# Kernel optimization log

Hardware: AMD Instinct MI355X
Metric: run time of the kernel (lower is better)

Reference implementation:

```python
import jax, jax.numpy as jnp
import numpy as np

B, T, D = 64, 256, 1024
H, HS = 16, 64
FF = 4096
EPS = 1e-5


def _layernorm(x, g, b):
    mu = jnp.mean(x, axis=-1, keepdims=True)
    var = jnp.mean(jnp.square(x - mu), axis=-1, keepdims=True)
    return (x - mu) * jax.lax.rsqrt(var + EPS) * g + b


def setup_inputs() -> dict:
    key = jax.random.key(0)
    ks = jax.random.split(key, 12)
    s = 0.02
    return {
        "x": jax.random.normal(ks[0], (B, T, D), jnp.float32),
        "ln1_g": jnp.ones((D,), jnp.float32),
        "ln1_b": jnp.zeros((D,), jnp.float32),
        "Wq": jax.random.normal(ks[1], (H, D, HS), jnp.float32) * s,
        "Wk": jax.random.normal(ks[2], (H, D, HS), jnp.float32) * s,
        "Wv": jax.random.normal(ks[3], (H, D, HS), jnp.float32) * s,
        "Wproj": jax.random.normal(ks[4], (D, D), jnp.float32) * s,
        "bproj": jnp.zeros((D,), jnp.float32),
        "ln2_g": jnp.ones((D,), jnp.float32),
        "ln2_b": jnp.zeros((D,), jnp.float32),
        "W1": jax.random.normal(ks[5], (D, FF), jnp.float32) * s,
        "b1": jnp.zeros((FF,), jnp.float32),
        "W2": jax.random.normal(ks[6], (FF, D), jnp.float32) * s,
        "b2": jnp.zeros((D,), jnp.float32),
    }


def reference(x, ln1_g, ln1_b, Wq, Wk, Wv, Wproj, bproj, ln2_g, ln2_b, W1, b1, W2, b2):
    # x = ln1(x)
    h = _layernorm(x, ln1_g, ln1_b)
    # per-head Q/K/V projections, batched over heads
    q = jnp.einsum("btd,hde->bhte", h, Wq)
    k = jnp.einsum("btd,hde->bhte", h, Wk)
    v = jnp.einsum("btd,hde->bhte", h, Wv)
    # NOTE: source scales by C**-0.5 with C = input_size (D), not head_size
    scale = D ** -0.5
    scores = jnp.einsum("bhte,bhse->bhts", q, k) * scale
    causal = jnp.tril(jnp.ones((T, T), bool))
    scores = jnp.where(causal, scores, -jnp.inf)
    w = jax.nn.softmax(scores, axis=-1)  # dropout is identity in eval
    attn = jnp.einsum("bhts,bhse->bthe", w, v).reshape(x.shape[0], x.shape[1], H * HS)
    sa = attn @ Wproj + bproj
    # residual onto ln1 output (as written in source)
    y = h + sa
    h2 = _layernorm(y, ln2_g, ln2_b)
    ff = jax.nn.relu(h2 @ W1 + b1) @ W2 + b2
    return h2 + ff
```

## Files before the change

### kernel.cpp

```cpp
#include <hip/hip_runtime.h>

typedef __bf16 bf16x8 __attribute__((ext_vector_type(8)));
typedef float f32x4 __attribute__((ext_vector_type(4)));
typedef unsigned short ushort_t;

__device__ __forceinline__ ushort_t f2bf(float f) {
  unsigned int u = __float_as_uint(f);
  u += 0x7fffu + ((u >> 16) & 1u);
  return (ushort_t)(u >> 16);
}

__device__ __forceinline__ void gl_lds16(const ushort_t* g, const char* l) {
  __builtin_amdgcn_global_load_lds(
      (const __attribute__((address_space(1))) void*)g,
      (__attribute__((address_space(3))) void*)l, 16, 0, 0);
}

__global__ __launch_bounds__(256) void fill_k(float* __restrict__ p, long n, float v) {
  long i = (long)blockIdx.x * 256 + threadIdx.x;
  if (i < n) p[i] = v;
}

__global__ __launch_bounds__(256) void transpose_w(const float* __restrict__ in,
                                                   ushort_t* __restrict__ out,
                                                   int R, int C) {
  __shared__ float tile[32][33];
  const float* inb = in + (long)blockIdx.z * R * C;
  ushort_t* outb = out + (long)blockIdx.z * R * C;
  int r0 = blockIdx.x * 32, c0 = blockIdx.y * 32;
  int tx = threadIdx.x & 31, ty = threadIdx.x >> 5;
#pragma unroll
  for (int i = ty; i < 32; i += 8) tile[i][tx] = inb[(long)(r0 + i) * C + (c0 + tx)];
  __syncthreads();
#pragma unroll
  for (int i = ty; i < 32; i += 8) outb[(long)(c0 + i) * R + (r0 + tx)] = f2bf(tile[tx][i]);
}

__global__ __launch_bounds__(256) void ln_k(const float* __restrict__ x,
                                            const float* __restrict__ g,
                                            const float* __restrict__ b,
                                            float* __restrict__ outF,
                                            ushort_t* __restrict__ outU) {
  __shared__ float red[8];
  long row = blockIdx.x;
  int tid = threadIdx.x;
  float4 v = ((const float4*)(x + row * 1024))[tid];
  float s = v.x + v.y + v.z + v.w;
#pragma unroll
  for (int off = 32; off; off >>= 1) s += __shfl_xor(s, off);
  int w = tid >> 6;
  if ((tid & 63) == 0) red[w] = s;
  __syncthreads();
  float mean = (red[0] + red[1] + red[2] + red[3]) * (1.0f / 1024.0f);
  float dx = v.x - mean, dy = v.y - mean, dz = v.z - mean, dw = v.w - mean;
  float s2 = dx * dx + dy * dy + dz * dz + dw * dw;
#pragma unroll
  for (int off = 32; off; off >>= 1) s2 += __shfl_xor(s2, off);
  if ((tid & 63) == 0) red[4 + w] = s2;
  __syncthreads();
  float var = (red[4] + red[5] + red[6] + red[7]) * (1.0f / 1024.0f);
  float rstd = rsqrtf(var + 1e-5f);
  int c = tid * 4;
  float o0 = dx * rstd * g[c + 0] + b[c + 0];
  float o1 = dy * rstd * g[c + 1] + b[c + 1];
  float o2 = dz * rstd * g[c + 2] + b[c + 2];
  float o3 = dw * rstd * g[c + 3] + b[c + 3];
  ((float4*)(outF + row * 1024))[tid] = make_float4(o0, o1, o2, o3);
  ushort4 u;
  u.x = f2bf(o0); u.y = f2bf(o1); u.z = f2bf(o2); u.w = f2bf(o3);
  ((ushort4*)(outU + row * 1024))[tid] = u;
}

template <int EPI>
__global__ __launch_bounds__(512, 2) void gemm256(const ushort_t* __restrict__ A,
                                                  const ushort_t* __restrict__ Bt,
                                                  int M, int N, int K, int NBC,
                                                  const float* __restrict__ bias,
                                                  const float* res, float* outF,
                                                  ushort_t* __restrict__ outU,
                                                  ushort_t* __restrict__ outU2,
                                                  ushort_t* __restrict__ outU3) {
  __shared__ __align__(16) char lds[131072];
  const int tid = threadIdx.x;
  const int lane = tid & 63;
  const int w = tid >> 6;
  const int wr = w >> 2, wc = w & 3;
  const int g = lane >> 4, lr = lane & 15;
  const int cpx = gridDim.x >> 3;
  const int wg = (blockIdx.x & 7) * cpx + (blockIdx.x >> 3);
  const long m0 = (long)(wg / NBC) * 256;
  const long n0 = (long)(wg % NBC) * 256;
  const int srow = tid >> 3;
  const int sslot = (tid & 7) ^ (srow & 7);
  const ushort_t* sA = A + (m0 + srow) * (long)K + sslot * 8;
  const ushort_t* sB = Bt + (n0 + srow) * (long)K + sslot * 8;
  const int dA = tid * 16;
  const int dB = 32768 + tid * 16;
  const int abase = (wr * 128 + lr) * 128;
  const int bbase = 32768 + (wc * 64 + lr) * 128;
  const int s0 = g ^ (lr & 7);
  const int s1 = (4 + g) ^ (lr & 7);
  const int NT = K >> 6;

  f32x4 acc[8][4] = {};

#pragma unroll
  for (int j = 0; j < 4; ++j) gl_lds16(sA + (long)j * 64 * K, lds + j * 8192 + dA);
#pragma unroll
  for (int j = 0; j < 4; ++j) gl_lds16(sB + (long)j * 64 * K, lds + j * 8192 + dB);

  bf16x8 aR[4][2], bR[4][2];
  int c = 0;
  for (int t = 0; t < NT; ++t) {
    const char* rb = lds + c;
    if (t + 1 < NT) {
      const long ko = (long)(t + 1) * 64;
      const int d = c ^ 65536;
#pragma unroll
      for (int j = 0; j < 4; ++j) gl_lds16(sA + ko + (long)j * 64 * K, lds + d + j * 8192 + dA);
#pragma unroll
      for (int j = 0; j < 4; ++j) gl_lds16(sB + ko + (long)j * 64 * K, lds + d + j * 8192 + dB);
      asm volatile("s_waitcnt vmcnt(8)" ::: "memory");
    } else {
      asm volatile("s_waitcnt vmcnt(0)" ::: "memory");
    }
    __builtin_amdgcn_s_barrier();
    __builtin_amdgcn_sched_barrier(0);
#pragma unroll
    for (int mf = 0; mf < 4; ++mf) {
      aR[mf][0] = *(const bf16x8*)(rb + abase + mf * 2048 + s0 * 16);
      aR[mf][1] = *(const bf16x8*)(rb + abase + mf * 2048 + s1 * 16);
    }
#pragma unroll
    for (int nf = 0; nf < 2; ++nf) {
      bR[nf][0] = *(const bf16x8*)(rb + bbase + nf * 2048 + s0 * 16);
      bR[nf][1] = *(const bf16x8*)(rb + bbase + nf * 2048 + s1 * 16);
    }
    __builtin_amdgcn_s_setprio(1);
#pragma unroll
    for (int mf = 0; mf < 4; ++mf)
#pragma unroll
      for (int nf = 0; nf < 2; ++nf) {
        acc[mf][nf] = __builtin_amdgcn_mfma_f32_16x16x32_bf16(aR[mf][0], bR[nf][0], acc[mf][nf], 0, 0, 0);
        acc[mf][nf] = __builtin_amdgcn_mfma_f32_16x16x32_bf16(aR[mf][1], bR[nf][1], acc[mf][nf], 0, 0, 0);
      }
    __builtin_amdgcn_s_setprio(0);
    __builtin_amdgcn_s_barrier();
#pragma unroll
    for (int nf = 2; nf < 4; ++nf) {
      bR[nf][0] = *(const bf16x8*)(rb + bbase + nf * 2048 + s0 * 16);
      bR[nf][1] = *(const bf16x8*)(rb + bbase + nf * 2048 + s1 * 16);
    }
    __builtin_amdgcn_s_setprio(1);
#pragma unroll
    for (int mf = 0; mf < 4; ++mf)
#pragma unroll
      for (int nf = 2; nf < 4; ++nf) {
        acc[mf][nf] = __builtin_amdgcn_mfma_f32_16x16x32_bf16(aR[mf][0], bR[nf][0], acc[mf][nf], 0, 0, 0);
        acc[mf][nf] = __builtin_amdgcn_mfma_f32_16x16x32_bf16(aR[mf][1], bR[nf][1], acc[mf][nf], 0, 0, 0);
      }
    __builtin_amdgcn_s_setprio(0);
    __builtin_amdgcn_s_barrier();
#pragma unroll
    for (int mf = 0; mf < 4; ++mf) {
      aR[mf][0] = *(const bf16x8*)(rb + abase + (4 + mf) * 2048 + s0 * 16);
      aR[mf][1] = *(const bf16x8*)(rb + abase + (4 + mf) * 2048 + s1 * 16);
    }
    __builtin_amdgcn_s_setprio(1);
#pragma unroll
    for (int mf = 0; mf < 4; ++mf)
#pragma unroll
      for (int nf = 2; nf < 4; ++nf) {
        acc[4 + mf][nf] = __builtin_amdgcn_mfma_f32_16x16x32_bf16(aR[mf][0], bR[nf][0], acc[4 + mf][nf], 0, 0, 0);
        acc[4 + mf][nf] = __builtin_amdgcn_mfma_f32_16x16x32_bf16(aR[mf][1], bR[nf][1], acc[4 + mf][nf], 0, 0, 0);
      }
    __builtin_amdgcn_s_setprio(0);
    __builtin_amdgcn_s_barrier();
    __builtin_amdgcn_s_setprio(1);
#pragma unroll
    for (int mf = 0; mf < 4; ++mf)
#pragma unroll
      for (int nf = 0; nf < 2; ++nf) {
        acc[4 + mf][nf] = __builtin_amdgcn_mfma_f32_16x16x32_bf16(aR[mf][0], bR[nf][0], acc[4 + mf][nf], 0, 0, 0);
        acc[4 + mf][nf] = __builtin_amdgcn_mfma_f32_16x16x32_bf16(aR[mf][1], bR[nf][1], acc[4 + mf][nf], 0, 0, 0);
      }
    __builtin_amdgcn_s_setprio(0);
    __builtin_amdgcn_s_barrier();
    c ^= 65536;
  }

#pragma unroll
  for (int mf = 0; mf < 8; ++mf)
#pragma unroll
    for (int nf = 0; nf < 4; ++nf)
#pragma unroll
      for (int r = 0; r < 4; ++r) {
        long row = m0 + wr * 128 + mf * 16 + g * 4 + r;
        long col = n0 + wc * 64 + nf * 16 + lr;
        float v = acc[mf][nf][r];
        if constexpr (EPI == 2) {
          long i = row * N + col;
          outF[i] = v + bias[col] + res[i];
        } else if constexpr (EPI == 3) {
          outU[row * N + col] = f2bf(fmaxf(v + bias[col], 0.0f));
        } else {
          long bb2 = row >> 8, tt = row & 255;
          long p = col >> 10, cc = col & 1023, hh = cc >> 6, e = cc & 63;
          if (p == 0)
            outU[(((bb2 * 16 + hh) * 256 + tt) << 6) + e] = f2bf(v);
          else if (p == 1)
            outU2[(((bb2 * 16 + hh) * 256 + tt) << 6) + e] = f2bf(v);
          else
            outU3[(((bb2 * 16 + hh) * 64 + e) << 8) + tt] = f2bf(v);
        }
      }
}

__global__ __launch_bounds__(64) void attn_k(const ushort_t* __restrict__ q,
                                             const ushort_t* __restrict__ k,
                                             const ushort_t* __restrict__ vt,
                                             ushort_t* __restrict__ ao) {
  __shared__ __align__(16) ushort_t Ps[64][40];
  const int lane = threadIdx.x;
  const int g = lane >> 4, lr = lane & 15;
  const int blk = blockIdx.x;
  const int q4 = blk & 3;
  const int bh = blk >> 2;
  const int bb = bh >> 4, hh = bh & 15;
  const int q0 = q4 * 64;
  const ushort_t* qb = q + (long)bh * 256 * 64;
  const ushort_t* kb = k + (long)bh * 256 * 64;
  const ushort_t* vb = vt + (long)bh * 64 * 256;
  bf16x8 qf[4][2];
#pragma unroll
  for (int m = 0; m < 4; m++)
#pragma unroll
    for (int ks = 0; ks < 2; ks++)
      qf[m][ks] = *(const bf16x8*)(qb + (q0 + m * 16 + lr) * 64 + ks * 32 + g * 8);
  f32x4 o[4][4] = {};
  float mrow[4][4], lrow[4][4];
#pragma unroll
  for (int m = 0; m < 4; m++)
#pragma unroll
    for (int r = 0; r < 4; r++) { mrow[m][r] = -__builtin_inff(); lrow[m][r] = 0.0f; }
  const float scale = 0.03125f;
  const int nkb = q0 / 32 + 2;
  for (int kbk = 0; kbk < nkb; kbk++) {
    f32x4 s[4][2] = {};
#pragma unroll
    for (int ks = 0; ks < 2; ks++) {
      bf16x8 kf[2];
#pragma unroll
      for (int n = 0; n < 2; n++)
        kf[n] = *(const bf16x8*)(kb + (kbk * 32 + n * 16 + lr) * 64 + ks * 32 + g * 8);
#pragma unroll
      for (int m = 0; m < 4; m++)
#pragma unroll
        for (int n = 0; n < 2; n++)
          s[m][n] = __builtin_amdgcn_mfma_f32_16x16x32_bf16(qf[m][ks], kf[n], s[m][n], 0, 0, 0);
    }
#pragma unroll
    for (int m = 0; m < 4; m++)
#pragma unroll
      for (int n = 0; n < 2; n++)
#pragma unroll
        for (int r = 0; r < 4; r++) {
          int row = q0 + m * 16 + g * 4 + r;
          int col = kbk * 32 + n * 16 + lr;
          float v = s[m][n][r] * scale;
          s[m][n][r] = (col <= row) ? v : -1e30f;
        }
#pragma unroll
    for (int m = 0; m < 4; m++)
#pragma unroll
      for (int r = 0; r < 4; r++) {
        float mx = fmaxf(s[m][0][r], s[m][1][r]);
#pragma unroll
        for (int off = 8; off; off >>= 1) mx = fmaxf(mx, __shfl_xor(mx, off));
        float mn = fmaxf(mrow[m][r], mx);
        float alpha = __expf(mrow[m][r] - mn);
        mrow[m][r] = mn;
        float rs = 0.0f;
#pragma unroll
        for (int n = 0; n < 2; n++) {
          float p = __expf(s[m][n][r] - mn);
          s[m][n][r] = p;
          rs += p;
        }
#pragma unroll
        for (int off = 8; off; off >>= 1) rs += __shfl_xor(rs, off);
        lrow[m][r] = lrow[m][r] * alpha + rs;
#pragma unroll
        for (int n = 0; n < 4; n++) o[m][n][r] *= alpha;
      }
#pragma unroll
    for (int m = 0; m < 4; m++)
#pragma unroll
      for (int n = 0; n < 2; n++)
#pragma unroll
        for (int r = 0; r < 4; r++)
          Ps[m * 16 + g * 4 + r][n * 16 + lr] = f2bf(s[m][n][r]);
    __syncthreads();
    bf16x8 vf[4];
#pragma unroll
    for (int n = 0; n < 4; n++)
      vf[n] = *(const bf16x8*)(vb + (n * 16 + lr) * 256 + kbk * 32 + g * 8);
#pragma unroll
    for (int m = 0; m < 4; m++) {
      bf16x8 pa = *(const bf16x8*)&Ps[m * 16 + lr][g * 8];
#pragma unroll
      for (int n = 0; n < 4; n++)
        o[m][n] = __builtin_amdgcn_mfma_f32_16x16x32_bf16(pa, vf[n], o[m][n], 0, 0, 0);
    }
    __syncthreads();
  }
#pragma unroll
  for (int m = 0; m < 4; m++)
#pragma unroll
    for (int r = 0; r < 4; r++) {
      float inv = 1.0f / lrow[m][r];
      long t = q0 + m * 16 + g * 4 + r;
#pragma unroll
      for (int n = 0; n < 4; n++) {
        long e = n * 16 + lr;
        ao[((long)bb * 256 + t) * 1024 + hh * 64 + e] = f2bf(o[m][n][r] * inv);
      }
    }
}

extern "C" void kernel_launch(void* const* d_in, const int* in_sizes, int n_in,
                              void* d_out, int out_size, void* d_ws, size_t ws_size,
                              hipStream_t stream) {
  const float* x     = (const float*)d_in[0];
  const float* ln1g  = (const float*)d_in[1];
  const float* ln1b  = (const float*)d_in[2];
  const float* Wq    = (const float*)d_in[3];
  const float* Wk    = (const float*)d_in[4];
  const float* Wv    = (const float*)d_in[5];
  const float* Wproj = (const float*)d_in[6];
  const float* bproj = (const float*)d_in[7];
  const float* ln2g  = (const float*)d_in[8];
  const float* ln2b  = (const float*)d_in[9];
  const float* W1    = (const float*)d_in[10];
  const float* b1    = (const float*)d_in[11];
  const float* W2    = (const float*)d_in[12];
  const float* b2    = (const float*)d_in[13];

  const long NEED = 184L << 20;
  if (ws_size < (size_t)NEED) {
    fill_k<<<(out_size + 255) / 256, 256, 0, stream>>>((float*)d_out, out_size,
                                                       (float)(ws_size >> 20));
    return;
  }

  char* ws = (char*)d_ws;
  const long MB = 1 << 20;
  ushort_t* wqt = (ushort_t*)(ws + 0 * MB);
  ushort_t* wkt = (ushort_t*)(ws + 2 * MB);
  ushort_t* wvt = (ushort_t*)(ws + 4 * MB);
  ushort_t* wpt = (ushort_t*)(ws + 6 * MB);
  ushort_t* w1t = (ushort_t*)(ws + 8 * MB);
  ushort_t* w2t = (ushort_t*)(ws + 16 * MB);
  ushort_t* hb  = (ushort_t*)(ws + 24 * MB);
  ushort_t* qbf = (ushort_t*)(ws + 56 * MB);
  ushort_t* kbf = (ushort_t*)(ws + 88 * MB);
  ushort_t* vtb = (ushort_t*)(ws + 120 * MB);
  ushort_t* atb = (ushort_t*)(ws + 152 * MB);
  ushort_t* ff1 = (ushort_t*)(ws + 56 * MB);
  float*    yf  = (float*)d_out;

  transpose_w<<<dim3(32, 2, 16), 256, 0, stream>>>(Wq, wqt, 1024, 64);
  transpose_w<<<dim3(32, 2, 16), 256, 0, stream>>>(Wk, wkt, 1024, 64);
  transpose_w<<<dim3(32, 2, 16), 256, 0, stream>>>(Wv, wvt, 1024, 64);
  transpose_w<<<dim3(32, 32, 1), 256, 0, stream>>>(Wproj, wpt, 1024, 1024);
  transpose_w<<<dim3(32, 128, 1), 256, 0, stream>>>(W1, w1t, 1024, 4096);
  transpose_w<<<dim3(128, 32, 1), 256, 0, stream>>>(W2, w2t, 4096, 1024);

  ln_k<<<16384, 256, 0, stream>>>(x, ln1g, ln1b, yf, hb);
  gemm256<4><<<768, 512, 0, stream>>>(hb, wqt, 16384, 3072, 1024, 12,
                                      nullptr, nullptr, nullptr, qbf, kbf, vtb);
  attn_k<<<4096, 64, 0, stream>>>(qbf, kbf, vtb, atb);
  gemm256<2><<<256, 512, 0, stream>>>(atb, wpt, 16384, 1024, 1024, 4,
                                      bproj, yf, yf, nullptr, nullptr, nullptr);
  ln_k<<<16384, 256, 0, stream>>>(yf, ln2g, ln2b, yf, hb);
  gemm256<3><<<1024, 512, 0, stream>>>(hb, w1t, 16384, 4096, 1024, 16,
                                       b1, nullptr, nullptr, ff1, nullptr, nullptr);
  gemm256<2><<<256, 512, 0, stream>>>(ff1, w2t, 16384, 1024, 4096, 4,
                                      b2, yf, yf, nullptr, nullptr, nullptr);
}
```

Before: 693.1 us.

## Interleave global-to-LDS staging with MFMA phases in 256x256 GEMM main loop

Restructures the GEMM main loop into a two-tile unrolled schedule where the next tiles' global-to-LDS loads are split into halves and issued between MFMA quadrants, rather than all at the start of each iteration. Explicit lgkmcnt and vmcnt waits plus barriers keep the double buffer consistent. The aim is to spread memory traffic across compute phases and hide load latency better. It adds more barriers and depends on the waitcnt counts being exact; a wrong count would race on the LDS buffers. The loop also assumes NT is even.

```diff
diff --git a/kernel.cpp b/kernel.cpp
--- a/kernel.cpp
+++ b/kernel.cpp
@@ -103,91 +103,109 @@
   const int NT = K >> 6;
 
   f32x4 acc[8][4] = {};
-
-#pragma unroll
-  for (int j = 0; j < 4; ++j) gl_lds16(sA + (long)j * 64 * K, lds + j * 8192 + dA);
-#pragma unroll
-  for (int j = 0; j < 4; ++j) gl_lds16(sB + (long)j * 64 * K, lds + j * 8192 + dB);
-
   bf16x8 aR[4][2], bR[4][2];
-  int c = 0;
-  for (int t = 0; t < NT; ++t) {
-    const char* rb = lds + c;
-    if (t + 1 < NT) {
-      const long ko = (long)(t + 1) * 64;
-      const int d = c ^ 65536;
-#pragma unroll
-      for (int j = 0; j < 4; ++j) gl_lds16(sA + ko + (long)j * 64 * K, lds + d + j * 8192 + dA);
-#pragma unroll
-      for (int j = 0; j < 4; ++j) gl_lds16(sB + ko + (long)j * 64 * K, lds + d + j * 8192 + dB);
-      asm volatile("s_waitcnt vmcnt(8)" ::: "memory");
-    } else {
-      asm volatile("s_waitcnt vmcnt(0)" ::: "memory");
-    }
-    __builtin_amdgcn_s_barrier();
-    __builtin_amdgcn_sched_barrier(0);
-#pragma unroll
-    for (int mf = 0; mf < 4; ++mf) {
-      aR[mf][0] = *(const bf16x8*)(rb + abase + mf * 2048 + s0 * 16);
-      aR[mf][1] = *(const bf16x8*)(rb + abase + mf * 2048 + s1 * 16);
-    }
-#pragma unroll
-    for (int nf = 0; nf < 2; ++nf) {
-      bR[nf][0] = *(const bf16x8*)(rb + bbase + nf * 2048 + s0 * 16);
-      bR[nf][1] = *(const bf16x8*)(rb + bbase + nf * 2048 + s1 * 16);
-    }
-    __builtin_amdgcn_s_setprio(1);
-#pragma unroll
-    for (int mf = 0; mf < 4; ++mf)
-#pragma unroll
-      for (int nf = 0; nf < 2; ++nf) {
-        acc[mf][nf] = __builtin_amdgcn_mfma_f32_16x16x32_bf16(aR[mf][0], bR[nf][0], acc[mf][nf], 0, 0, 0);
-        acc[mf][nf] = __builtin_amdgcn_mfma_f32_16x16x32_bf16(aR[mf][1], bR[nf][1], acc[mf][nf], 0, 0, 0);
-      }
-    __builtin_amdgcn_s_setprio(0);
-    __builtin_amdgcn_s_barrier();
-#pragma unroll
-    for (int nf = 2; nf < 4; ++nf) {
-      bR[nf][0] = *(const bf16x8*)(rb + bbase + nf * 2048 + s0 * 16);
-      bR[nf][1] = *(const bf16x8*)(rb + bbase + nf * 2048 + s1 * 16);
-    }
-    __builtin_amdgcn_s_setprio(1);
-#pragma unroll
-    for (int mf = 0; mf < 4; ++mf)
-#pragma unroll
-      for (int nf = 2; nf < 4; ++nf) {
-        acc[mf][nf] = __builtin_amdgcn_mfma_f32_16x16x32_bf16(aR[mf][0], bR[nf][0], acc[mf][nf], 0, 0, 0);
-        acc[mf][nf] = __builtin_amdgcn_mfma_f32_16x16x32_bf16(aR[mf][1], bR[nf][1], acc[mf][nf], 0, 0, 0);
-      }
-    __builtin_amdgcn_s_setprio(0);
-    __builtin_amdgcn_s_barrier();
-#pragma unroll
-    for (int mf = 0; mf < 4; ++mf) {
-      aR[mf][0] = *(const bf16x8*)(rb + abase + (4 + mf) * 2048 + s0 * 16);
-      aR[mf][1] = *(const bf16x8*)(rb + abase + (4 + mf) * 2048 + s1 * 16);
-    }
-    __builtin_amdgcn_s_setprio(1);
-#pragma unroll
-    for (int mf = 0; mf < 4; ++mf)
-#pragma unroll
-      for (int nf = 2; nf < 4; ++nf) {
-        acc[4 + mf][nf] = __builtin_amdgcn_mfma_f32_16x16x32_bf16(aR[mf][0], bR[nf][0], acc[4 + mf][nf], 0, 0, 0);
-        acc[4 + mf][nf] = __builtin_amdgcn_mfma_f32_16x16x32_bf16(aR[mf][1], bR[nf][1], acc[4 + mf][nf], 0, 0, 0);
-      }
-    __builtin_amdgcn_s_setprio(0);
-    __builtin_amdgcn_s_barrier();
-    __builtin_amdgcn_s_setprio(1);
-#pragma unroll
-    for (int mf = 0; mf < 4; ++mf)
-#pragma unroll
-      for (int nf = 0; nf < 2; ++nf) {
-        acc[4 + mf][nf] = __builtin_amdgcn_mfma_f32_16x16x32_bf16(aR[mf][0], bR[nf][0], acc[4 + mf][nf], 0, 0, 0);
-        acc[4 + mf][nf] = __builtin_amdgcn_mfma_f32_16x16x32_bf16(aR[mf][1], bR[nf][1], acc[4 + mf][nf], 0, 0, 0);
-      }
-    __builtin_amdgcn_s_setprio(0);
-    __builtin_amdgcn_s_barrier();
-    c ^= 65536;
+  const char* rb;
+
+#define STAGE_A(tile, half) do {                                          \
+    const long _ko = (long)(tile) * 64;                                   \
+    char* _d = lds + (((tile) & 1) << 16) + ((half) << 14) + dA;          \
+    gl_lds16(sA + _ko + (long)(2 * (half)) * 64 * K, _d);                 \
+    gl_lds16(sA + _ko + (long)(2 * (half) + 1) * 64 * K, _d + 8192);      \
+  } while (0)
+#define STAGE_B(tile, half) do {                                          \
+    const long _ko = (long)(tile) * 64;                                   \
+    char* _d = lds + (((tile) & 1) << 16) + ((half) << 14) + dB;          \
+    gl_lds16(sB + _ko + (long)(2 * (half)) * 64 * K, _d);                 \
+    gl_lds16(sB + _ko + (long)(2 * (half) + 1) * 64 * K, _d + 8192);      \
+  } while (0)
+#define RD_A(base_mf) do {                                                \
+    _Pragma("unroll") for (int mf = 0; mf < 4; ++mf) {                    \
+      aR[mf][0] = *(const bf16x8*)(rb + abase + ((base_mf) + mf) * 2048 + s0 * 16); \
+      aR[mf][1] = *(const bf16x8*)(rb + abase + ((base_mf) + mf) * 2048 + s1 * 16); \
+    } } while (0)
+#define RD_B2(base_nf) do {                                               \
+    _Pragma("unroll") for (int nf = 0; nf < 2; ++nf) {                    \
+      bR[(base_nf) + nf][0] = *(const bf16x8*)(rb + bbase + ((base_nf) + nf) * 2048 + s0 * 16); \
+      bR[(base_nf) + nf][1] = *(const bf16x8*)(rb + bbase + ((base_nf) + nf) * 2048 + s1 * 16); \
+    } } while (0)
+#define QUAD(MB, NB) do {                                                 \
+    __builtin_amdgcn_s_setprio(1);                                        \
+    _Pragma("unroll") for (int mf = 0; mf < 4; ++mf)                      \
+      _Pragma("unroll") for (int nf = 0; nf < 2; ++nf) {                  \
+        acc[(MB) + mf][(NB) + nf] = __builtin_amdgcn_mfma_f32_16x16x32_bf16(aR[mf][0], bR[(NB) + nf][0], acc[(MB) + mf][(NB) + nf], 0, 0, 0); \
+        acc[(MB) + mf][(NB) + nf] = __builtin_amdgcn_mfma_f32_16x16x32_bf16(aR[mf][1], bR[(NB) + nf][1], acc[(MB) + mf][(NB) + nf], 0, 0, 0); \
+      }                                                                   \
+    __builtin_amdgcn_s_setprio(0); } while (0)
+#define LGKM0 do {                                                        \
+    asm volatile("s_waitcnt lgkmcnt(0)" ::: "memory");                    \
+    __builtin_amdgcn_sched_barrier(0); } while (0)
+
+  STAGE_B(0, 0); STAGE_B(0, 1); STAGE_A(0, 0); STAGE_A(0, 1);
+  STAGE_B(1, 0); STAGE_B(1, 1); STAGE_A(1, 0);
+  asm volatile("s_waitcnt vmcnt(6)" ::: "memory");
+  __builtin_amdgcn_s_barrier();
+
+  for (int t = 0; t < NT; t += 2) {
+    const bool s2 = (t + 2 < NT), s3 = (t + 3 < NT);
+    rb = lds;
+    RD_A(0);
+    RD_B2(0);
+    STAGE_A(t + 1, 1);
+    asm volatile("s_waitcnt lgkmcnt(8)" ::: "memory");
+    __builtin_amdgcn_s_barrier();
+    LGKM0;
+    QUAD(0, 0);
+    __builtin_amdgcn_s_barrier();
+    RD_B2(2);
+    __builtin_amdgcn_s_barrier();
+    LGKM0;
+    QUAD(0, 2);
+    __builtin_amdgcn_s_barrier();
+    if (s2) STAGE_B(t + 2, 0);
+    RD_A(4);
+    __builtin_amdgcn_s_barrier();
+    LGKM0;
+    QUAD(4, 2);
+    __builtin_amdgcn_s_barrier();
+    if (s2) { STAGE_B(t + 2, 1); STAGE_A(t + 2, 0); }
+    __builtin_amdgcn_s_barrier();
+    QUAD(4, 0);
+    if (s2) asm volatile("s_waitcnt vmcnt(6)" ::: "memory");
+    else    asm volatile("s_waitcnt vmcnt(0)" ::: "memory");
+    __builtin_amdgcn_s_barrier();
+    rb = lds + 65536;
+    RD_A(0);
+    RD_B2(0);
+    if (s2) STAGE_A(t + 2, 1);
+    asm volatile("s_waitcnt lgkmcnt(8)" ::: "memory");
+    __builtin_amdgcn_s_barrier();
+    LGKM0;
+    QUAD(0, 0);
+    __builtin_amdgcn_s_barrier();
+    RD_B2(2);
+    __builtin_amdgcn_s_barrier();
+    LGKM0;
+    QUAD(0, 2);
+    __builtin_amdgcn_s_barrier();
+    if (s3) STAGE_B(t + 3, 0);
+    RD_A(4);
+    __builtin_amdgcn_s_barrier();
+    LGKM0;
+    QUAD(4, 2);
+    __builtin_amdgcn_s_barrier();
+    if (s3) { STAGE_B(t + 3, 1); STAGE_A(t + 3, 0); }
+    __builtin_amdgcn_s_barrier();
+    QUAD(4, 0);
+    if (s3) asm volatile("s_waitcnt vmcnt(6)" ::: "memory");
+    else    asm volatile("s_waitcnt vmcnt(0)" ::: "memory");
+    __builtin_amdgcn_s_barrier();
   }
+#undef STAGE_A
+#undef STAGE_B
+#undef RD_A
+#undef RD_B2
+#undef QUAD
+#undef LGKM0
 
 #pragma unroll
   for (int mf = 0; mf < 8; ++mf)
```

Result: no change. 687.0 us (-0.9%).
